# Performance work log

Measured on AMD Instinct MI355X. Metric: run time of the kernel, lower is better.

Reference implementation:

```python
import jax, jax.numpy as jnp
import numpy as np

M, IN_F, OUT_F = 8192, 4096, 4096
A_N, A_K = 64, 64  # out_factor1, in_factor1
B_N, B_K = 64, 64  # out_factor2, in_factor2


def setup_inputs() -> dict:
    key = jax.random.key(0)
    k1, k2, k3, k4 = jax.random.split(key, 4)
    x = jax.random.normal(k1, (M, IN_F), dtype=jnp.float32)
    A = jax.random.normal(k2, (A_N, A_K), dtype=jnp.float32) * 0.05
    B = jax.random.normal(k3, (B_N, B_K), dtype=jnp.float32) * 0.05
    bias = jax.random.normal(k4, (OUT_F,), dtype=jnp.float32) * 0.02
    return {"x": x, "A": A, "B": B, "bias": bias}


def reference(x, A, B, bias):
    # out = x @ kron(A, B).T + bias, computed without materializing kron(A,B).
    m = x.shape[0]
    x3 = x.reshape(m, A_K, B_K)                 # [M, A_K, B_K]
    tmp = jnp.einsum('mkl,pk->mpl', x3, A)      # contract A_K -> A_N
    out = jnp.einsum('mpl,ql->mpq', tmp, B)     # contract B_K -> B_N
    return out.reshape(m, A_N * B_N) + bias
```

## Files before the change

### kernel.cpp

```cpp
#include <hip/hip_runtime.h>
#include <hip/hip_bf16.h>


typedef __bf16 bf16x8 __attribute__((ext_vector_type(8)));
typedef __bf16 bf16x4 __attribute__((ext_vector_type(4)));
typedef float  f32x4  __attribute__((ext_vector_type(4)));

#define MFMA16(Aop, Bop, C) __builtin_amdgcn_mfma_f32_16x16x32_bf16(Aop, Bop, C, 0, 0, 0)

__device__ __forceinline__ bf16x8 load_cvt8(const float* __restrict__ p) {
    const float4 a = *reinterpret_cast<const float4*>(p);
    const float4 b = *reinterpret_cast<const float4*>(p + 4);
    bf16x8 r;
    r[0] = (__bf16)a.x; r[1] = (__bf16)a.y; r[2] = (__bf16)a.z; r[3] = (__bf16)a.w;
    r[4] = (__bf16)b.x; r[5] = (__bf16)b.y; r[6] = (__bf16)b.z; r[7] = (__bf16)b.w;
    return r;
}

__global__ __launch_bounds__(256, 4)
void kron_linear_kernel(const float* __restrict__ x,
                        const float* __restrict__ A,
                        const float* __restrict__ B,
                        const float* __restrict__ bias,
                        float* __restrict__ out) {
    __shared__ __align__(16) char Ulds[4][8192];

    const int lane = threadIdx.x & 63;
    const int wv   = threadIdx.x >> 6;
    const int lr   = lane & 15;
    const int hi   = lane >> 4;
    const int m    = blockIdx.x * 4 + wv;

    char* ubase = &Ulds[wv][0];
    const float* xrow = x + (size_t)m * 4096;

    bf16x8 Af[4][2], Bf[4][2];
    #pragma unroll
    for (int t = 0; t < 4; ++t) {
        #pragma unroll
        for (int kt = 0; kt < 2; ++kt) {
            const int row = 16 * t + lr;
            const int c0  = 32 * kt + 8 * hi;
            Af[t][kt] = load_cvt8(A + row * 64 + c0);
            Bf[t][kt] = load_cvt8(B + row * 64 + c0);
        }
    }

    bf16x8 Xf[4][2];
    #pragma unroll
    for (int mt = 0; mt < 4; ++mt) {
        #pragma unroll
        for (int kt = 0; kt < 2; ++kt) {
            Xf[mt][kt] = load_cvt8(xrow + (16 * mt + lr) * 64 + 32 * kt + 8 * hi);
        }
    }

    #pragma unroll
    for (int mt = 0; mt < 4; ++mt) {
        #pragma unroll
        for (int nt = 0; nt < 4; ++nt) {
            f32x4 u = {0.f, 0.f, 0.f, 0.f};
            u = MFMA16(Xf[mt][0], Bf[nt][0], u);
            u = MFMA16(Xf[mt][1], Bf[nt][1], u);
            const int q   = 16 * nt + lr;
            const int k0  = 16 * mt + 4 * hi;
            const int off = (q * 128 + k0 * 2) ^ ((q & 7) << 4);
            bf16x4 v;
            v[0] = (__bf16)u[0];
            v[1] = (__bf16)u[1];
            v[2] = (__bf16)u[2];
            v[3] = (__bf16)u[3];
            *reinterpret_cast<bf16x4*>(ubase + off) = v;
        }
    }

    asm volatile("s_waitcnt lgkmcnt(0)" ::: "memory");

    bf16x8 Uf[2][4];
    #pragma unroll
    for (int kt = 0; kt < 2; ++kt) {
        #pragma unroll
        for (int qt = 0; qt < 4; ++qt) {
            const int q   = 16 * qt + lr;
            const int k0  = 32 * kt + 8 * hi;
            const int off = (q * 128 + k0 * 2) ^ ((q & 7) << 4);
            Uf[kt][qt] = *reinterpret_cast<const bf16x8*>(ubase + off);
        }
    }

    asm volatile("s_waitcnt lgkmcnt(0)" ::: "memory");

    float* orow = out + (size_t)m * 4096;
    #pragma unroll
    for (int h = 0; h < 2; ++h) {
        #pragma unroll
        for (int ptl = 0; ptl < 2; ++ptl) {
            const int pt = 2 * h + ptl;
            #pragma unroll
            for (int qt = 0; qt < 4; ++qt) {
                f32x4 acc = {0.f, 0.f, 0.f, 0.f};
                acc = MFMA16(Uf[0][qt], Af[pt][0], acc);
                acc = MFMA16(Uf[1][qt], Af[pt][1], acc);
                const int pp  = 16 * ptl + lr;
                const int q0  = 16 * qt + 4 * hi;
                const int off = (pp * 256 + q0 * 4) ^ ((pp & 7) << 4);
                *reinterpret_cast<f32x4*>(ubase + off) = acc;
            }
        }
        asm volatile("s_waitcnt lgkmcnt(0)" ::: "memory");

        #pragma unroll
        for (int i = 0; i < 8; ++i) {
            const int pp  = 4 * i + hi;
            const int off = (i * 1024 + lane * 16) ^ ((pp & 7) << 4);
            const f32x4 v = *reinterpret_cast<const f32x4*>(ubase + off);
            const int col = 2048 * h + i * 256 + lane * 4;
            const f32x4 bv = *reinterpret_cast<const f32x4*>(bias + col);
            f32x4 o;
            o[0] = v[0] + bv[0];
            o[1] = v[1] + bv[1];
            o[2] = v[2] + bv[2];
            o[3] = v[3] + bv[3];
            __builtin_nontemporal_store(o, reinterpret_cast<f32x4*>(orow + col));
        }
        asm volatile("s_waitcnt lgkmcnt(0)" ::: "memory");
    }
}

extern "C" void kernel_launch(void* const* d_in, const int* in_sizes, int n_in,
                              void* d_out, int out_size, void* d_ws, size_t ws_size,
                              hipStream_t stream) {
    const float* x    = (const float*)d_in[0];
    const float* A    = (const float*)d_in[1];
    const float* B    = (const float*)d_in[2];
    const float* bias = (const float*)d_in[3];
    float* out        = (float*)d_out;

    kron_linear_kernel<<<dim3(2048), dim3(256), 0, stream>>>(x, A, B, bias, out);
}
```

Before: 70.00 us.

## Process two rows per wave and prefetch next row's x during compute

Each wave now handles two consecutive output rows, halving the grid. It issues raw float4 loads for the second row before computing the first, so the memory latency overlaps with the first row's MFMA, LDS and store work, and the A/B fragment loads are amortised over two rows. The 16 float4 prefetch registers raise register pressure, so the launch-bounds occupancy hint drops from 4 to 3 blocks per SIMD. Fewer waves in flight may reduce latency hiding from occupancy on a memory-bound kernel.

```diff
diff --git a/kernel.cpp b/kernel.cpp
--- a/kernel.cpp
+++ b/kernel.cpp
@@ -17,41 +17,23 @@
     return r;
 }
 
-__global__ __launch_bounds__(256, 4)
-void kron_linear_kernel(const float* __restrict__ x,
-                        const float* __restrict__ A,
-                        const float* __restrict__ B,
-                        const float* __restrict__ bias,
-                        float* __restrict__ out) {
-    __shared__ __align__(16) char Ulds[4][8192];
-
-    const int lane = threadIdx.x & 63;
-    const int wv   = threadIdx.x >> 6;
-    const int lr   = lane & 15;
-    const int hi   = lane >> 4;
-    const int m    = blockIdx.x * 4 + wv;
-
-    char* ubase = &Ulds[wv][0];
-    const float* xrow = x + (size_t)m * 4096;
-
-    bf16x8 Af[4][2], Bf[4][2];
-    #pragma unroll
-    for (int t = 0; t < 4; ++t) {
+template<bool PRE>
+__device__ __forceinline__
+void do_row(const int m, bf16x8 (&Xf)[4][2],
+            const bf16x8 (&Af)[4][2], const bf16x8 (&Bf)[4][2],
+            char* ubase, const float* __restrict__ xnext,
+            const float* __restrict__ bias, float* __restrict__ out,
+            const int lane, const int lr, const int hi) {
+    float4 pre[16];
+    if (PRE) {
         #pragma unroll
-        for (int kt = 0; kt < 2; ++kt) {
-            const int row = 16 * t + lr;
-            const int c0  = 32 * kt + 8 * hi;
-            Af[t][kt] = load_cvt8(A + row * 64 + c0);
-            Bf[t][kt] = load_cvt8(B + row * 64 + c0);
-        }
-    }
-
-    bf16x8 Xf[4][2];
-    #pragma unroll
-    for (int mt = 0; mt < 4; ++mt) {
-        #pragma unroll
-        for (int kt = 0; kt < 2; ++kt) {
-            Xf[mt][kt] = load_cvt8(xrow + (16 * mt + lr) * 64 + 32 * kt + 8 * hi);
+        for (int mt = 0; mt < 4; ++mt) {
+            #pragma unroll
+            for (int kt = 0; kt < 2; ++kt) {
+                const float* p = xnext + (16 * mt + lr) * 64 + 32 * kt + 8 * hi;
+                pre[(mt * 2 + kt) * 2]     = *reinterpret_cast<const float4*>(p);
+                pre[(mt * 2 + kt) * 2 + 1] = *reinterpret_cast<const float4*>(p + 4);
+            }
         }
     }
 
@@ -125,6 +107,66 @@
         }
         asm volatile("s_waitcnt lgkmcnt(0)" ::: "memory");
     }
+
+    if (PRE) {
+        #pragma unroll
+        for (int mt = 0; mt < 4; ++mt) {
+            #pragma unroll
+            for (int kt = 0; kt < 2; ++kt) {
+                const float4 a = pre[(mt * 2 + kt) * 2];
+                const float4 b = pre[(mt * 2 + kt) * 2 + 1];
+                bf16x8 r;
+                r[0] = (__bf16)a.x; r[1] = (__bf16)a.y;
+                r[2] = (__bf16)a.z; r[3] = (__bf16)a.w;
+                r[4] = (__bf16)b.x; r[5] = (__bf16)b.y;
+                r[6] = (__bf16)b.z; r[7] = (__bf16)b.w;
+                Xf[mt][kt] = r;
+            }
+        }
+    }
+}
+
+__global__ __launch_bounds__(256, 3)
+void kron_linear_kernel(const float* __restrict__ x,
+                        const float* __restrict__ A,
+                        const float* __restrict__ B,
+                        const float* __restrict__ bias,
+                        float* __restrict__ out) {
+    __shared__ __align__(16) char Ulds[4][8192];
+
+    const int lane = threadIdx.x & 63;
+    const int wv   = threadIdx.x >> 6;
+    const int lr   = lane & 15;
+    const int hi   = lane >> 4;
+    const int m0   = (blockIdx.x * 4 + wv) * 2;
+
+    char* ubase = &Ulds[wv][0];
+
+    bf16x8 Af[4][2], Bf[4][2];
+    #pragma unroll
+    for (int t = 0; t < 4; ++t) {
+        #pragma unroll
+        for (int kt = 0; kt < 2; ++kt) {
+            const int row = 16 * t + lr;
+            const int c0  = 32 * kt + 8 * hi;
+            Af[t][kt] = load_cvt8(A + row * 64 + c0);
+            Bf[t][kt] = load_cvt8(B + row * 64 + c0);
+        }
+    }
+
+    const float* xrow0 = x + (size_t)m0 * 4096;
+    bf16x8 Xf[4][2];
+    #pragma unroll
+    for (int mt = 0; mt < 4; ++mt) {
+        #pragma unroll
+        for (int kt = 0; kt < 2; ++kt) {
+            Xf[mt][kt] = load_cvt8(xrow0 + (16 * mt + lr) * 64 + 32 * kt + 8 * hi);
+        }
+    }
+
+    const float* xrow1 = xrow0 + 4096;
+    do_row<true >(m0,     Xf, Af, Bf, ubase, xrow1, bias, out, lane, lr, hi);
+    do_row<false>(m0 + 1, Xf, Af, Bf, ubase, xrow1, bias, out, lane, lr, hi);
 }
 
 extern "C" void kernel_launch(void* const* d_in, const int* in_sizes, int n_in,
@@ -136,5 +178,5 @@
     const float* bias = (const float*)d_in[3];
     float* out        = (float*)d_out;
 
-    kron_linear_kernel<<<dim3(2048), dim3(256), 0, stream>>>(x, A, B, bias, out);
+    kron_linear_kernel<<<dim3(1024), dim3(256), 0, stream>>>(x, A, B, bias, out);
 }
```

After: 98.94 us. 1.41x slower.
